# Kernel tuning notes

Hardware: AMD Instinct MI355X
Metric: run time of the kernel (lower is better)

## Reference

```python
import jax, jax.numpy as jnp
import numpy as np

L, B, N, D, H, DH, MLP = 4, 4, 2048, 512, 8, 64, 2048
EPS = 1e-5


def layer_norm(x, w, b):
    mu = jnp.mean(x, axis=-1, keepdims=True)
    var = jnp.mean(jnp.square(x - mu), axis=-1, keepdims=True)
    return (x - mu) * jax.lax.rsqrt(var + EPS) * w + b


def setup_inputs() -> dict:
    key = jax.random.key(0)
    ks = jax.random.split(key, 8)
    x = jax.random.normal(ks[0], (B, N, D), dtype=jnp.float32)
    # mask == 1.0 means blocked: triu(ones) - eye -> strict upper triangle
    mask = jnp.triu(jnp.ones((N, N), dtype=jnp.float32)) - jnp.eye(N, dtype=jnp.float32)
    s = 0.02
    return {
        "x": x,
        "mask": mask,
        "ln1_w": jnp.ones((L, D), jnp.float32),
        "ln1_b": jnp.zeros((L, D), jnp.float32),
        "w_qkv": jax.random.normal(ks[1], (L, D, 3 * H * DH), jnp.float32) * s,
        "w_out": jax.random.normal(ks[2], (L, H * DH, D), jnp.float32) * s,
        "b_out": jnp.zeros((L, D), jnp.float32),
        "ln2_w": jnp.ones((L, D), jnp.float32),
        "ln2_b": jnp.zeros((L, D), jnp.float32),
        "w1": jax.random.normal(ks[3], (L, D, MLP), jnp.float32) * s,
        "b1": jnp.zeros((L, MLP), jnp.float32),
        "w2": jax.random.normal(ks[4], (L, MLP, D), jnp.float32) * s,
        "b2": jnp.zeros((L, D), jnp.float32),
    }


def reference(x, mask, ln1_w, ln1_b, w_qkv, w_out, b_out, ln2_w, ln2_b, w1, b1, w2, b2):
    scale = DH ** (-0.5)
    blocked = (mask == 1.0)  # [N, N]
    for l in range(L):
        # --- masked self-attention (pre-norm) ---
        h = layer_norm(x, ln1_w[l], ln1_b[l])
        qkv = h @ w_qkv[l]                               # [B, N, 3*H*DH]
        q, k, v = jnp.split(qkv, 3, axis=-1)
        q = q.reshape(B, N, H, DH).transpose(0, 2, 1, 3)  # bhnd
        k = k.reshape(B, N, H, DH).transpose(0, 2, 1, 3)
        v = v.reshape(B, N, H, DH).transpose(0, 2, 1, 3)
        scores = jnp.einsum('bhnd,bhmd->bhnm', q, k) * scale
        scores = jnp.where(blocked, -jnp.inf, scores)
        att = jax.nn.softmax(scores, axis=-1)
        o = jnp.einsum('bhnm,bhmd->bhnd', att, v)
        o = o.transpose(0, 2, 1, 3).reshape(B, N, H * DH)
        x = x + (o @ w_out[l] + b_out[l])
        # --- GELU MLP (pre-norm) ---
        h2 = layer_norm(x, ln2_w[l], ln2_b[l])
        ff = jax.nn.gelu(h2 @ w1[l] + b1[l], approximate=False) @ w2[l] + b2[l]
        x = x + ff
    return x
```

## Files before the change

### kernel.cpp

```cpp
#include <hip/hip_runtime.h>
#include <math.h>

#define L 4
#define BATCH 4
#define N 2048
#define D 512
#define H 8
#define DH 64
#define MLPD 2048
#define M_ROWS (BATCH * N)
#define VTP 2064

using v8s = __attribute__((ext_vector_type(8))) short;
using v4f = __attribute__((ext_vector_type(4))) float;

__device__ inline short f2bf(float f) {
  union { float f; unsigned u; } v; v.f = f;
  unsigned r = v.u + 0x7FFFu + ((v.u >> 16) & 1u);
  return (short)(r >> 16);
}
__device__ inline unsigned pack2bf_t(float a, float b) {
  union { float f; unsigned u; } x, y; x.f = a; y.f = b;
  return (x.u >> 16) | (y.u & 0xFFFF0000u);
}

#define MFMA(a, b, c) __builtin_amdgcn_mfma_f32_16x16x32_bf16(a, b, c, 0, 0, 0)

__device__ __forceinline__ void gload_lds16(const void* g, void* l) {
  __builtin_amdgcn_global_load_lds((const __attribute__((address_space(1))) void*)g,
                                   (__attribute__((address_space(3))) void*)l, 16, 0, 0);
}

#define FENCE asm volatile("" ::: "memory")
#define BAR  do { FENCE; __builtin_amdgcn_s_barrier(); FENCE; } while (0)
#define VMW(n) asm volatile("s_waitcnt vmcnt(" #n ")" ::: "memory")

__global__ void copyf4_kernel(const float4* __restrict__ in, float4* __restrict__ out, int n) {
  int i = blockIdx.x * blockDim.x + threadIdx.x;
  if (i < n) out[i] = in[i];
}

__launch_bounds__(256)
__global__ void transpose_w_kernel(const float* __restrict__ src, short* __restrict__ dst,
                                   int R, int C, int qcols) {
  __shared__ float tile[32][33];
  const size_t base = (size_t)blockIdx.z * R * C;
  const int c0 = blockIdx.x * 32, r0 = blockIdx.y * 32;
  const int tx = threadIdx.x & 31, ty = threadIdx.x >> 5;
  #pragma unroll
  for (int i = ty; i < 32; i += 8)
    tile[i][tx] = src[base + (size_t)(r0 + i) * C + c0 + tx];
  __syncthreads();
  #pragma unroll
  for (int i = ty; i < 32; i += 8) {
    float val = tile[tx][i];
    if (c0 + i < qcols) val *= 0.125f;
    dst[base + (size_t)(c0 + i) * R + r0 + tx] = f2bf(val);
  }
}

__launch_bounds__(256)
__global__ void ln_kernel(const float* __restrict__ x, const float* __restrict__ w,
                          const float* __restrict__ b, short* __restrict__ out) {
  const int row = blockIdx.x * 4 + (threadIdx.x >> 6);
  const int lane = threadIdx.x & 63;
  const float* xr = x + (size_t)row * D;
  float4 a0 = *(const float4*)(xr + lane * 8);
  float4 a1 = *(const float4*)(xr + lane * 8 + 4);
  float v[8] = {a0.x, a0.y, a0.z, a0.w, a1.x, a1.y, a1.z, a1.w};
  float s = 0.f;
  #pragma unroll
  for (int j = 0; j < 8; ++j) s += v[j];
  #pragma unroll
  for (int m = 1; m < 64; m <<= 1) s += __shfl_xor(s, m, 64);
  const float mean = s * (1.0f / D);
  float q = 0.f;
  #pragma unroll
  for (int j = 0; j < 8; ++j) { float d = v[j] - mean; q += d * d; }
  #pragma unroll
  for (int m = 1; m < 64; m <<= 1) q += __shfl_xor(q, m, 64);
  const float rstd = rsqrtf(q * (1.0f / D) + 1e-5f);
  float4 w0 = *(const float4*)(w + lane * 8);
  float4 w1 = *(const float4*)(w + lane * 8 + 4);
  float4 b0 = *(const float4*)(b + lane * 8);
  float4 b1 = *(const float4*)(b + lane * 8 + 4);
  float wv[8] = {w0.x, w0.y, w0.z, w0.w, w1.x, w1.y, w1.z, w1.w};
  float bv[8] = {b0.x, b0.y, b0.z, b0.w, b1.x, b1.y, b1.z, b1.w};
  v8s r;
  #pragma unroll
  for (int j = 0; j < 8; ++j) r[j] = f2bf((v[j] - mean) * rstd * wv[j] + bv[j]);
  *(v8s*)(out + (size_t)row * D + lane * 8) = r;
}

template <int MODE, int NT>
__launch_bounds__(512, 2)
__global__ void gemm256_kernel(const short* __restrict__ A, const short* __restrict__ Bt,
                               const float* __restrict__ bias, void* __restrict__ Out,
                               int M, int Nc) {
  constexpr int K = NT * 64;
  __shared__ __align__(16) short Ah[4][128 * 64];
  __shared__ __align__(16) short Bh[4][128 * 64];
  const int tid = threadIdx.x, lane = tid & 63, w = tid >> 6;
  const int wr = w >> 2, wc = w & 3;
  const int r16 = lane & 15, g = lane >> 4;

  const int nxb = Nc >> 8;
  const int nyb = M >> 8;
  const int bid = (int)blockIdx.x;
  const int xcd = bid & 7, ii = bid >> 3;
  const int byi = xcd * (nyb >> 3) + ii / nxb;
  const int bxi = ii % nxb;
  const int m0 = byi << 8, n0 = bxi << 8;

  const int srow = lane >> 3;
  const int ssw = ((lane & 7) ^ srow) * 8;

  const short* Abase = A + (size_t)(m0 + srow) * K + ssw;
  const short* Bbase = Bt + (size_t)(n0 + srow) * K + ssw;

  auto STAGE_A = [&](int j) {
    if (j >= 2 * NT) return;
    const int slot = j & 3, k0 = (j >> 1) * 64, r0 = (j & 1) * 128;
    #pragma unroll
    for (int i = 0; i < 2; ++i) {
      const int rr = i * 64 + w * 8;
      gload_lds16(Abase + (size_t)(r0 + rr) * K + k0, (char*)&Ah[slot][0] + rr * 128);
    }
  };
  auto STAGE_B = [&](int j) {
    if (j >= 2 * NT) return;
    const int slot = j & 3, k0 = (j >> 1) * 64, c0 = (j & 1) * 128;
    #pragma unroll
    for (int i = 0; i < 2; ++i) {
      const int rr = i * 64 + w * 8;
      gload_lds16(Bbase + (size_t)(c0 + rr) * K + k0, (char*)&Bh[slot][0] + rr * 128);
    }
  };

  const int arow = wr * 64 + r16;
  const int brow = wc * 32 + r16;
  const int swz7 = r16 & 7;

  v8s ar[4][2], br0[2][2], br1[2][2];
  auto LDA = [&](int slot) {
    const char* base = (const char*)&Ah[slot][0];
    #pragma unroll
    for (int mf = 0; mf < 4; ++mf)
      #pragma unroll
      for (int kh = 0; kh < 2; ++kh)
        ar[mf][kh] = *(const v8s*)(base + (arow + mf * 16) * 128 + (((kh * 4 + g) ^ swz7) * 16));
  };
  auto LDB0 = [&](int slot) {
    const char* base = (const char*)&Bh[slot][0];
    #pragma unroll
    for (int nf = 0; nf < 2; ++nf)
      #pragma unroll
      for (int kh = 0; kh < 2; ++kh)
        br0[nf][kh] = *(const v8s*)(base + (brow + nf * 16) * 128 + (((kh * 4 + g) ^ swz7) * 16));
  };
  auto LDB1 = [&](int slot) {
    const char* base = (const char*)&Bh[slot][0];
    #pragma unroll
    for (int nf = 0; nf < 2; ++nf)
      #pragma unroll
      for (int kh = 0; kh < 2; ++kh)
        br1[nf][kh] = *(const v8s*)(base + (brow + nf * 16) * 128 + (((kh * 4 + g) ^ swz7) * 16));
  };

  v4f acc[2][2][4][2] = {};

#define MMA_Q(QM, QN, BR)                                                      \
  do {                                                                         \
    __builtin_amdgcn_s_setprio(1);                                             \
    _Pragma("unroll")                                                          \
    for (int kh = 0; kh < 2; ++kh)                                             \
      _Pragma("unroll")                                                        \
      for (int mf = 0; mf < 4; ++mf)                                           \
        _Pragma("unroll")                                                      \
        for (int nf = 0; nf < 2; ++nf)                                         \
          acc[QM][QN][mf][nf] = MFMA(ar[mf][kh], BR[nf][kh], acc[QM][QN][mf][nf]); \
    __builtin_amdgcn_s_setprio(0);                                             \
  } while (0)

  STAGE_A(0); STAGE_B(0); STAGE_B(1); STAGE_A(1); STAGE_A(2); STAGE_B(2); STAGE_B(3);
  VMW(6);
  BAR;

  auto KTILE = [&](int T, int sa) {
    LDA(sa); LDB0(sa);
    STAGE_A(2 * T + 3);
    BAR;
    MMA_Q(0, 0, br0);
    BAR;
    LDB1(sa + 1);
    BAR;
    MMA_Q(0, 1, br1);
    BAR;
    LDA(sa + 1);
    STAGE_A(2 * T + 4); STAGE_B(2 * T + 4);
    BAR;
    MMA_Q(1, 1, br1);
    BAR;
    STAGE_B(2 * T + 5);
    BAR;
    MMA_Q(1, 0, br0);
    VMW(4);
    BAR;
  };

  #pragma unroll
  for (int t2 = 0; t2 < NT / 2; ++t2) {
    KTILE(2 * t2, 0);
    KTILE(2 * t2 + 1, 2);
  }
#undef MMA_Q

  #pragma unroll
  for (int qm = 0; qm < 2; ++qm)
    #pragma unroll
    for (int mf = 0; mf < 4; ++mf) {
      const int row = m0 + qm * 128 + wr * 64 + mf * 16 + g * 4;
      #pragma unroll
      for (int qn = 0; qn < 2; ++qn)
        #pragma unroll
        for (int nf = 0; nf < 2; ++nf) {
          const int col = n0 + qn * 128 + wc * 32 + nf * 16 + r16;
          float bv = 0.0f;
          if constexpr (MODE == 1) bv = bias[col];
          #pragma unroll
          for (int r = 0; r < 4; ++r) {
            float val = acc[qm][qn][mf][nf][r] + bv;
            if constexpr (MODE == 1) {
              const float z = val * 0.70710678118f;
              const float az = fabsf(z);
              const float t = 1.0f / (1.0f + 0.3275911f * az);
              const float p =
                  0.254829592f +
                  t * (-0.284496736f + t * (1.421413741f + t * (-1.453152027f + t * 1.061405429f)));
              float er = 1.0f - p * t * __expf(-az * az);
              er = (z < 0.0f) ? -er : er;
              val = 0.5f * val * (1.0f + er);
            }
            ((short*)Out)[(size_t)(row + r) * Nc + col] = f2bf(val);
          }
        }
    }
}

template <int MODE, int BN>
__launch_bounds__(256)
__global__ void gemm128_kernel(const short* __restrict__ A, const short* __restrict__ Bt,
                               const float* __restrict__ bias, const float* __restrict__ Xres,
                               void* __restrict__ Out, int M, int Nc, int K) {
  constexpr int MR = (BN == 128) ? 4 : 2;
  __shared__ __align__(16) short As[2][128 * 64];
  __shared__ __align__(16) short Bs[2][BN * 64];
  const int tid = threadIdx.x;
  const int lane = tid & 63;
  const int w = tid >> 6;
  const int wr = (BN == 128) ? (w >> 1) : w;
  const int wc = (BN == 128) ? (w & 1) : 0;
  const int r16 = lane & 15, g = lane >> 4;

  const int nxb = Nc / BN;
  const int nyb = M >> 7;
  const int bid = (int)blockIdx.x;
  const int xcd = bid & 7;
  const int ii = bid >> 3;
  const int byi = xcd * (nyb >> 3) + ii / nxb;
  const int bxi = ii % nxb;
  const int m0 = byi * 128, n0 = bxi * BN;

  const int srow = lane >> 3;
  const int ssw = ((lane & 7) ^ srow) * 8;

  auto STAGE = [&](int buf, int k0) {
    #pragma unroll
    for (int j = 0; j < 4; ++j) {
      const int row = w * 32 + j * 8;
      gload_lds16(A + (size_t)(m0 + row + srow) * K + k0 + ssw,
                  (char*)&As[buf][0] + row * 128);
    }
    #pragma unroll
    for (int j = 0; j < BN / 32; ++j) {
      const int row = w * (BN / 4) + j * 8;
      gload_lds16(Bt + (size_t)(n0 + row + srow) * K + k0 + ssw,
                  (char*)&Bs[buf][0] + row * 128);
    }
  };

  v4f acc[MR][4] = {};

  STAGE(0, 0);
  __syncthreads();
  int cur = 0;
  for (int k0 = 0; k0 < K; k0 += 64) {
    if (k0 + 64 < K) STAGE(cur ^ 1, k0 + 64);
    v8s af[MR][2], bf[4][2];
    #pragma unroll
    for (int m = 0; m < MR; ++m) {
      const int row = wr * (MR * 16) + m * 16 + r16;
      #pragma unroll
      for (int kh = 0; kh < 2; ++kh)
        af[m][kh] = *(const v8s*)((const char*)&As[cur][0] + row * 128 +
                                  (((kh * 4 + g) ^ (row & 7)) * 16));
    }
    #pragma unroll
    for (int n = 0; n < 4; ++n) {
      const int row = wc * 64 + n * 16 + r16;
      #pragma unroll
      for (int kh = 0; kh < 2; ++kh)
        bf[n][kh] = *(const v8s*)((const char*)&Bs[cur][0] + row * 128 +
                                  (((kh * 4 + g) ^ (row & 7)) * 16));
    }
    #pragma unroll
    for (int kh = 0; kh < 2; ++kh)
      #pragma unroll
      for (int m = 0; m < MR; ++m)
        #pragma unroll
        for (int n = 0; n < 4; ++n)
          acc[m][n] = MFMA(af[m][kh], bf[n][kh], acc[m][n]);
    __syncthreads();
    cur ^= 1;
  }

  #pragma unroll
  for (int m = 0; m < MR; ++m) {
    const int row = m0 + wr * (MR * 16) + m * 16 + g * 4;
    #pragma unroll
    for (int n = 0; n < 4; ++n) {
      const int col = n0 + wc * 64 + n * 16 + r16;
      const float bv = bias ? bias[col] : 0.0f;
      #pragma unroll
      for (int r = 0; r < 4; ++r) {
        const size_t idx = (size_t)(row + r) * Nc + col;
        float val = acc[m][n][r] + bv;
        if constexpr (MODE == 0) {
          ((short*)Out)[idx] = f2bf(val);
        } else if constexpr (MODE == 1) {
          const float z = val * 0.70710678118f;
          const float az = fabsf(z);
          const float t = 1.0f / (1.0f + 0.3275911f * az);
          const float p =
              0.254829592f +
              t * (-0.284496736f + t * (1.421413741f + t * (-1.453152027f + t * 1.061405429f)));
          float er = 1.0f - p * t * __expf(-az * az);
          er = (z < 0.0f) ? -er : er;
          val = 0.5f * val * (1.0f + er);
          ((short*)Out)[idx] = f2bf(val);
        } else {
          ((float*)Out)[idx] = val + Xres[idx];
        }
      }
    }
  }
}

__launch_bounds__(256)
__global__ void kv_prep_kernel(const short* __restrict__ qkv, short* __restrict__ Vt) {
  __shared__ __align__(16) short tile[64][88];
  const int b = blockIdx.z, h = blockIdx.y, n0 = blockIdx.x * 64;
  const int tid = threadIdx.x;
  const int bh = b * H + h;
  const int row2 = tid >> 3, d0 = (tid & 7) * 8;
  #pragma unroll
  for (int i = 0; i < 2; ++i) {
    const int n = i * 32 + row2;
    const short* src = qkv + ((size_t)(b * N + n0 + n)) * 1536 + 1024 + h * 64 + d0;
    *(v8s*)&tile[n][d0] = *(const v8s*)src;
  }
  __syncthreads();
  const int dh = tid & 63, nc = (tid >> 6) * 16;
  #pragma unroll
  for (int j = 0; j < 2; ++j) {
    const int oc = nc + j * 8;
    const int base = (oc >> 5) * 32 + ((oc >> 3) & 3) * 4;
    v8s ov;
    #pragma unroll
    for (int e = 0; e < 4; ++e) ov[e] = tile[base + e][dh];
    #pragma unroll
    for (int e = 0; e < 4; ++e) ov[4 + e] = tile[base + 16 + e][dh];
    *(v8s*)(Vt + ((size_t)(bh * 64 + dh)) * VTP + n0 + oc) = ov;
  }
}

__launch_bounds__(256)
__global__ void attn_kernel(const short* __restrict__ qkv, const short* __restrict__ Vt,
                            short* __restrict__ o) {
  __shared__ __align__(16) short Ks[3][64 * 64];
  __shared__ __align__(16) short Vs[2][64 * 64];
  const int lin = (int)blockIdx.x;
  const int bh = ((lin >> 3) & 3) * 8 + (lin & 7);
  const int xl2 = 31 - (lin >> 5);
  const int b = bh >> 3, h = bh & 7;
  const int q0 = xl2 * 64;
  const int tid = threadIdx.x, lane = tid & 63, w = tid >> 6;
  const int r16 = lane & 15, g = lane >> 4;
  const int qw = q0 + w * 16;

  v8s qf0, qf1;
  {
    const size_t qbase = ((size_t)(b * N + qw + r16)) * 1536 + h * 64;
    qf0 = *(const v8s*)(qkv + qbase + g * 8);
    qf1 = *(const v8s*)(qkv + qbase + 32 + g * 8);
  }

  const short* vtb = Vt + (size_t)bh * 64 * VTP;

  const int srow = lane >> 3;
  const int ssw = ((lane & 7) ^ srow) * 8;

  v4f oacc[4] = {};
  float lsum = 0.f;
  const int tdiag = xl2;

  auto STAGE_K = [&](int t) {
    t = (t > tdiag) ? tdiag : t;
    const int k0 = t * 64, buf = t % 3;
    #pragma unroll
    for (int j = 0; j < 2; ++j) {
      const int row = w * 16 + j * 8;
      gload_lds16(qkv + ((size_t)(b * N + k0 + row + srow)) * 1536 + 512 + h * 64 + ssw,
                  (char*)&Ks[buf][0] + row * 128);
    }
  };
  auto STAGE_V = [&](int t) {
    t = (t > tdiag) ? tdiag : t;
    const int k0 = t * 64, buf = t & 1;
    #pragma unroll
    for (int j = 0; j < 2; ++j) {
      const int row = w * 16 + j * 8;
      gload_lds16(vtb + (size_t)(row + srow) * VTP + k0 + ssw,
                  (char*)&Vs[buf][0] + row * 128);
    }
  };

  STAGE_K(0); STAGE_V(0); STAGE_K(1);

  for (int t = 0; t <= tdiag; ++t) {
    VMW(2);
    BAR;
    STAGE_V(t + 1);
    STAGE_K(t + 2);

    const char* kb = (const char*)&Ks[t % 3][0];
    const char* vb = (const char*)&Vs[t & 1][0];

    v8s vf[4][2];
    #pragma unroll
    for (int a = 0; a < 4; ++a)
      #pragma unroll
      for (int c = 0; c < 2; ++c)
        vf[a][c] = *(const v8s*)(vb + (a * 16 + r16) * 128 + (((c * 4 + g) ^ (r16 & 7)) * 16));

    __builtin_amdgcn_s_setprio(1);
    v4f s[4];
    #pragma unroll
    for (int kt = 0; kt < 4; ++kt) {
      const int krow = (kt * 16 + r16) * 128;
      v8s kfa = *(const v8s*)(kb + krow + ((g ^ (r16 & 7)) * 16));
      v8s kfb = *(const v8s*)(kb + krow + (((4 + g) ^ (r16 & 7)) * 16));
      v4f ss = {};
      ss = MFMA(kfa, qf0, ss);
      ss = MFMA(kfb, qf1, ss);
      s[kt] = ss;
    }
    __builtin_amdgcn_s_setprio(0);

    const bool needmask = (t == tdiag);
    const int qrow = qw + r16;
    const int kbase = t * 64 + 4 * g;
    unsigned pw_[8];
    #pragma unroll
    for (int kt = 0; kt < 4; ++kt) {
      float e[4];
      #pragma unroll
      for (int r = 0; r < 4; ++r) {
        float v = s[kt][r];
        if (needmask && (kbase + kt * 16 + r > qrow)) v = -3e38f;
        e[r] = __expf(v);
      }
      lsum += (e[0] + e[1]) + (e[2] + e[3]);
      pw_[kt * 2 + 0] = pack2bf_t(e[0], e[1]);
      pw_[kt * 2 + 1] = pack2bf_t(e[2], e[3]);
    }
    union PU { unsigned u[4]; v8s s8; };
    PU pa0, pa1;
    pa0.u[0] = pw_[0]; pa0.u[1] = pw_[1]; pa0.u[2] = pw_[2]; pa0.u[3] = pw_[3];
    pa1.u[0] = pw_[4]; pa1.u[1] = pw_[5]; pa1.u[2] = pw_[6]; pa1.u[3] = pw_[7];

    __builtin_amdgcn_s_setprio(1);
    #pragma unroll
    for (int dt = 0; dt < 4; ++dt) oacc[dt] = MFMA(pa0.s8, vf[dt][0], oacc[dt]);
    #pragma unroll
    for (int dt = 0; dt < 4; ++dt) oacc[dt] = MFMA(pa1.s8, vf[dt][1], oacc[dt]);
    __builtin_amdgcn_s_setprio(0);
  }

  lsum += __shfl_xor(lsum, 16, 64);
  lsum += __shfl_xor(lsum, 32, 64);
  float ldiv[4];
  #pragma unroll
  for (int r = 0; r < 4; ++r) ldiv[r] = __shfl(lsum, g * 4 + r, 64);

  #pragma unroll
  for (int dt = 0; dt < 4; ++dt)
    #pragma unroll
    for (int r = 0; r < 4; ++r) {
      const float val = oacc[dt][r] / ldiv[r];
      o[((size_t)(b * N + qw + g * 4 + r)) * 512 + h * 64 + dt * 16 + r16] = f2bf(val);
    }
}

extern "C" void kernel_launch(void* const* d_in, const int* in_sizes, int n_in,
                              void* d_out, int out_size, void* d_ws, size_t ws_size,
                              hipStream_t stream) {
  const float* x_in  = (const float*)d_in[0];
  const float* ln1_w = (const float*)d_in[2];
  const float* ln1_b = (const float*)d_in[3];
  const float* w_qkv = (const float*)d_in[4];
  const float* w_out = (const float*)d_in[5];
  const float* b_out = (const float*)d_in[6];
  const float* ln2_w = (const float*)d_in[7];
  const float* ln2_b = (const float*)d_in[8];
  const float* w1    = (const float*)d_in[9];
  const float* b1    = (const float*)d_in[10];
  const float* w2    = (const float*)d_in[11];
  const float* b2    = (const float*)d_in[12];

  char* ws = (char*)d_ws;
  size_t off = 0;
  auto alloc = [&](size_t bytes) { char* p = ws + off; off += (bytes + 255) & ~(size_t)255; return p; };
  short* wqkvT = (short*)alloc((size_t)L * 1536 * 512 * 2);
  short* woutT = (short*)alloc((size_t)L * 512 * 512 * 2);
  short* w1T   = (short*)alloc((size_t)L * 512 * 2048 * 2);
  short* w2T   = (short*)alloc((size_t)L * 2048 * 512 * 2);
  short* hln   = (short*)alloc((size_t)M_ROWS * 512 * 2);
  short* big   = (short*)alloc((size_t)M_ROWS * 2048 * 2);
  short* oatt  = (short*)alloc((size_t)M_ROWS * 512 * 2);
  short* Vtg   = (short*)alloc((size_t)BATCH * H * 64 * VTP * 2);
  short* qkv = big;
  short* ff  = big;

  float* x = (float*)d_out;

  copyf4_kernel<<<4096, 256, 0, stream>>>((const float4*)x_in, (float4*)x, M_ROWS * D / 4);

  transpose_w_kernel<<<dim3(1536 / 32, 512 / 32, L), 256, 0, stream>>>(w_qkv, wqkvT, 512, 1536, 512);
  transpose_w_kernel<<<dim3(512 / 32, 512 / 32, L), 256, 0, stream>>>(w_out, woutT, 512, 512, 0);
  transpose_w_kernel<<<dim3(2048 / 32, 512 / 32, L), 256, 0, stream>>>(w1, w1T, 512, 2048, 0);
  transpose_w_kernel<<<dim3(512 / 32, 2048 / 32, L), 256, 0, stream>>>(w2, w2T, 2048, 512, 0);

  for (int l = 0; l < L; ++l) {
    ln_kernel<<<M_ROWS / 4, 256, 0, stream>>>(x, ln1_w + l * 512, ln1_b + l * 512, hln);
    gemm256_kernel<0, 8><<<dim3((1536 / 256) * (M_ROWS / 256)), 512, 0, stream>>>(
        hln, wqkvT + (size_t)l * 1536 * 512, nullptr, qkv, M_ROWS, 1536);
    kv_prep_kernel<<<dim3(N / 64, H, BATCH), 256, 0, stream>>>(qkv, Vtg);
    attn_kernel<<<dim3(1024), 256, 0, stream>>>(qkv, Vtg, oatt);
    gemm128_kernel<2, 64><<<dim3((512 / 64) * (M_ROWS / 128)), 256, 0, stream>>>(
        oatt, woutT + (size_t)l * 512 * 512, b_out + l * 512, x, x, M_ROWS, 512, 512);
    ln_kernel<<<M_ROWS / 4, 256, 0, stream>>>(x, ln2_w + l * 512, ln2_b + l * 512, hln);
    gemm256_kernel<1, 8><<<dim3((2048 / 256) * (M_ROWS / 256)), 512, 0, stream>>>(
        hln, w1T + (size_t)l * 512 * 2048, b1 + l * 2048, ff, M_ROWS, 2048);
    gemm128_kernel<2, 64><<<dim3((512 / 64) * (M_ROWS / 128)), 256, 0, stream>>>(
        ff, w2T + (size_t)l * 2048 * 512, b2 + l * 512, x, x, M_ROWS, 512, 2048);
  }
}
```

Baseline: 627.5 us.

## Fuse V transpose into QKV GEMM epilogue and drop kv_prep kernel

The QKV GEMM gets a new mode that writes V-column tiles straight into the transposed, permuted Vt layout from accumulators, removing the separate kv_prep launch and its extra read and write of V. The GEMM prologue staging now clamps out-of-range stages (redundant loads instead of early return) with a changed vmcnt wait, keeping the wait count uniform. Attention normalisation uses one reciprocal and multiplies instead of dividing. Risks include strided 8-byte scattered stores in the epilogue and the correctness of the permutation mapping.

```diff
diff --git a/kernel.cpp b/kernel.cpp
--- a/kernel.cpp
+++ b/kernel.cpp
@@ -96,7 +96,7 @@
 __launch_bounds__(512, 2)
 __global__ void gemm256_kernel(const short* __restrict__ A, const short* __restrict__ Bt,
                                const float* __restrict__ bias, void* __restrict__ Out,
-                               int M, int Nc) {
+                               short* __restrict__ Vt, int M, int Nc) {
   constexpr int K = NT * 64;
   __shared__ __align__(16) short Ah[4][128 * 64];
   __shared__ __align__(16) short Bh[4][128 * 64];
@@ -119,8 +119,8 @@
   const short* Bbase = Bt + (size_t)(n0 + srow) * K + ssw;
 
   auto STAGE_A = [&](int j) {
-    if (j >= 2 * NT) return;
-    const int slot = j & 3, k0 = (j >> 1) * 64, r0 = (j & 1) * 128;
+    const int jc = (j > 2 * NT - 1) ? (2 * NT - 1) : j;
+    const int slot = j & 3, k0 = (jc >> 1) * 64, r0 = (jc & 1) * 128;
     #pragma unroll
     for (int i = 0; i < 2; ++i) {
       const int rr = i * 64 + w * 8;
@@ -128,8 +128,8 @@
     }
   };
   auto STAGE_B = [&](int j) {
-    if (j >= 2 * NT) return;
-    const int slot = j & 3, k0 = (j >> 1) * 64, c0 = (j & 1) * 128;
+    const int jc = (j > 2 * NT - 1) ? (2 * NT - 1) : j;
+    const int slot = j & 3, k0 = (jc >> 1) * 64, c0 = (jc & 1) * 128;
     #pragma unroll
     for (int i = 0; i < 2; ++i) {
       const int rr = i * 64 + w * 8;
@@ -204,7 +204,7 @@
     STAGE_B(2 * T + 5);
     BAR;
     MMA_Q(1, 0, br0);
-    VMW(4);
+    VMW(6);
     BAR;
   };
 
@@ -215,6 +215,38 @@
   }
 #undef MMA_Q
 
+  if constexpr (MODE == 3) {
+    if (n0 >= 1024) {
+      const int bb = m0 >> 11;
+      const int cperm = 16 * (g >> 1) + 8 * (g & 1);
+      #pragma unroll
+      for (int qm = 0; qm < 2; ++qm)
+        #pragma unroll
+        for (int mf = 0; mf < 4; ++mf) {
+          const int key0 = m0 + qm * 128 + wr * 64 + mf * 16;
+          const int ng = (key0 & 2047) & ~63;
+          const int c = ((key0 & 63) & 32) + cperm + 32 * (mf >> 1) % 32;
+          const int ccol = 32 * (mf >> 1) + cperm + 4 * (mf & 1);
+          (void)c;
+          #pragma unroll
+          for (int qn = 0; qn < 2; ++qn)
+            #pragma unroll
+            for (int nf = 0; nf < 2; ++nf) {
+              const int col = n0 + qn * 128 + wc * 32 + nf * 16 + r16;
+              const int dhg = col - 1024;
+              const int bh = bb * 8 + (dhg >> 6);
+              short* dst = Vt + (size_t)(bh * 64 + (dhg & 63)) * VTP + ng + ccol;
+              uint2 st;
+              st.x = (unsigned)(unsigned short)f2bf(acc[qm][qn][mf][nf][0]) |
+                     ((unsigned)(unsigned short)f2bf(acc[qm][qn][mf][nf][1]) << 16);
+              st.y = (unsigned)(unsigned short)f2bf(acc[qm][qn][mf][nf][2]) |
+                     ((unsigned)(unsigned short)f2bf(acc[qm][qn][mf][nf][3]) << 16);
+              *(uint2*)dst = st;
+            }
+        }
+      return;
+    }
+  }
   #pragma unroll
   for (int qm = 0; qm < 2; ++qm)
     #pragma unroll
@@ -357,34 +389,6 @@
 }
 
 __launch_bounds__(256)
-__global__ void kv_prep_kernel(const short* __restrict__ qkv, short* __restrict__ Vt) {
-  __shared__ __align__(16) short tile[64][88];
-  const int b = blockIdx.z, h = blockIdx.y, n0 = blockIdx.x * 64;
-  const int tid = threadIdx.x;
-  const int bh = b * H + h;
-  const int row2 = tid >> 3, d0 = (tid & 7) * 8;
-  #pragma unroll
-  for (int i = 0; i < 2; ++i) {
-    const int n = i * 32 + row2;
-    const short* src = qkv + ((size_t)(b * N + n0 + n)) * 1536 + 1024 + h * 64 + d0;
-    *(v8s*)&tile[n][d0] = *(const v8s*)src;
-  }
-  __syncthreads();
-  const int dh = tid & 63, nc = (tid >> 6) * 16;
-  #pragma unroll
-  for (int j = 0; j < 2; ++j) {
-    const int oc = nc + j * 8;
-    const int base = (oc >> 5) * 32 + ((oc >> 3) & 3) * 4;
-    v8s ov;
-    #pragma unroll
-    for (int e = 0; e < 4; ++e) ov[e] = tile[base + e][dh];
-    #pragma unroll
-    for (int e = 0; e < 4; ++e) ov[4 + e] = tile[base + 16 + e][dh];
-    *(v8s*)(Vt + ((size_t)(bh * 64 + dh)) * VTP + n0 + oc) = ov;
-  }
-}
-
-__launch_bounds__(256)
 __global__ void attn_kernel(const short* __restrict__ qkv, const short* __restrict__ Vt,
                             short* __restrict__ o) {
   __shared__ __align__(16) short Ks[3][64 * 64];
@@ -499,15 +503,16 @@
 
   lsum += __shfl_xor(lsum, 16, 64);
   lsum += __shfl_xor(lsum, 32, 64);
+  const float linv = 1.0f / lsum;
   float ldiv[4];
   #pragma unroll
-  for (int r = 0; r < 4; ++r) ldiv[r] = __shfl(lsum, g * 4 + r, 64);
+  for (int r = 0; r < 4; ++r) ldiv[r] = __shfl(linv, g * 4 + r, 64);
 
   #pragma unroll
   for (int dt = 0; dt < 4; ++dt)
     #pragma unroll
     for (int r = 0; r < 4; ++r) {
-      const float val = oacc[dt][r] / ldiv[r];
+      const float val = oacc[dt][r] * ldiv[r];
       o[((size_t)(b * N + qw + g * 4 + r)) * 512 + h * 64 + dt * 16 + r16] = f2bf(val);
     }
 }
@@ -553,15 +558,14 @@
 
   for (int l = 0; l < L; ++l) {
     ln_kernel<<<M_ROWS / 4, 256, 0, stream>>>(x, ln1_w + l * 512, ln1_b + l * 512, hln);
-    gemm256_kernel<0, 8><<<dim3((1536 / 256) * (M_ROWS / 256)), 512, 0, stream>>>(
-        hln, wqkvT + (size_t)l * 1536 * 512, nullptr, qkv, M_ROWS, 1536);
-    kv_prep_kernel<<<dim3(N / 64, H, BATCH), 256, 0, stream>>>(qkv, Vtg);
+    gemm256_kernel<3, 8><<<dim3((1536 / 256) * (M_ROWS / 256)), 512, 0, stream>>>(
+        hln, wqkvT + (size_t)l * 1536 * 512, nullptr, qkv, Vtg, M_ROWS, 1536);
     attn_kernel<<<dim3(1024), 256, 0, stream>>>(qkv, Vtg, oatt);
     gemm128_kernel<2, 64><<<dim3((512 / 64) * (M_ROWS / 128)), 256, 0, stream>>>(
         oatt, woutT + (size_t)l * 512 * 512, b_out + l * 512, x, x, M_ROWS, 512, 512);
     ln_kernel<<<M_ROWS / 4, 256, 0, stream>>>(x, ln2_w + l * 512, ln2_b + l * 512, hln);
     gemm256_kernel<1, 8><<<dim3((2048 / 256) * (M_ROWS / 256)), 512, 0, stream>>>(
-        hln, w1T + (size_t)l * 512 * 2048, b1 + l * 2048, ff, M_ROWS, 2048);
+        hln, w1T + (size_t)l * 512 * 2048, b1 + l * 2048, ff, nullptr, M_ROWS, 2048);
     gemm128_kernel<2, 64><<<dim3((512 / 64) * (M_ROWS / 128)), 256, 0, stream>>>(
         ff, w2T + (size_t)l * 2048 * 512, b2 + l * 512, x, x, M_ROWS, 512, 2048);
   }
```

New measurement: 604.7 us. 3.6% less time.
